# Kernel optimization log

Measured on AMD Instinct MI355X. Metric: run time of the kernel, lower is better.

## Reference

```python
import jax, jax.numpy as jnp
import numpy as np

K = 3          # B-spline order (cubic)
G = 10         # number of spline intervals over [0, 1]
NELY, NELX = 512, 512
WIDTHS = [2, 32, 32, 1]


def _make_grid(in_dim):
    # extended uniform knot vector over [0,1] with K extra knots each side: (in_dim, G+2K+1)
    h = 1.0 / G
    knots = jnp.arange(-K, G + K + 1, dtype=jnp.float32) * h
    return jnp.tile(knots[None, :], (in_dim, 1))


def setup_inputs() -> dict:
    key = jax.random.key(0)
    ks = jax.random.split(key, 1 + 3 * (len(WIDTHS) - 1))
    inp = {"coords": jax.random.uniform(ks[0], (NELY * NELX, 2), dtype=jnp.float32)}
    for l, (i, o) in enumerate(zip(WIDTHS[:-1], WIDTHS[1:])):
        inp[f"grid{l}"] = _make_grid(i)
        inp[f"coef{l}"] = 0.1 * jax.random.normal(ks[1 + 3 * l], (i, o, G + K), dtype=jnp.float32)
        inp[f"sb{l}"] = jax.random.normal(ks[2 + 3 * l], (i, o), dtype=jnp.float32) / np.sqrt(i).astype(np.float32)
        inp[f"sp{l}"] = jnp.ones((i, o), dtype=jnp.float32)
    inp["density_bias"] = jnp.full((1,), np.float32(np.log(0.5 / (1.0 - 0.5 + 1e-8))))
    return inp


def _b_batch(x, grid):
    # Cox-de Boor recursion. x: (B, in), grid: (in, G+2K+1) -> bases (B, in, G+K)
    xe = x[:, :, None]
    v = ((xe >= grid[None, :, :-1]) & (xe < grid[None, :, 1:])).astype(x.dtype)
    for p in range(1, K + 1):
        left = (xe - grid[None, :, : -(p + 1)]) / (grid[None, :, p:-1] - grid[None, :, : -(p + 1)])
        right = (grid[None, :, p + 1:] - xe) / (grid[None, :, p + 1:] - grid[None, :, 1:-p])
        v = left * v[:, :, :-1] + right * v[:, :, 1:]
    return v


def _kan_layer(x, grid, coef, sb, sp):
    # y_out = sum_in [ sb * silu(x) + sp * sum_k B_k(x) * coef_k ]
    B = _b_batch(x, grid)                               # (batch, in, G+K)
    spline = jnp.einsum('bik,iok->bio', B, coef)        # (batch, in, out)
    base = jax.nn.silu(x)                               # (batch, in)
    return jnp.sum(sb[None] * base[:, :, None] + sp[None] * spline, axis=1)


def reference(coords, grid0, coef0, sb0, sp0, grid1, coef1, sb1, sp1,
              grid2, coef2, sb2, sp2, density_bias):
    h = _kan_layer(coords, grid0, coef0, sb0, sp0)
    h = _kan_layer(h, grid1, coef1, sb1, sp1)
    logits = _kan_layer(h, grid2, coef2, sb2, sp2) + density_bias
    return jax.nn.sigmoid(logits).reshape(1, NELY, NELX)
```

## Files before the change

### kernel.cpp

```cpp
#include <hip/hip_runtime.h>
#include <hip/hip_bf16.h>

typedef __hip_bfloat16 bf16;
typedef __fp16 h2v __attribute__((ext_vector_type(2)));
typedef __fp16 half8 __attribute__((ext_vector_type(8)));
typedef float floatx4 __attribute__((ext_vector_type(4)));

#define NPTS (512*512)

#define OFF_BIAS 12
#define OFF_FLAG 13
#define OFF_BF   16
#define NFRAG    50
#define WS_WORDS (16 + NFRAG*64*4)


__device__ __forceinline__ bool sniff_f32(const void* g0) {
    float f = ((const float*)g0)[0];
    return fabsf(f + 0.3f) < 0.01f;
}
__device__ __forceinline__ float ld(const void* p, int i, bool f32) {
    return f32 ? ((const float*)p)[i] : __bfloat162float(((const bf16*)p)[i]);
}
__device__ __forceinline__ unsigned pk_rtn(float a, float b) {
    union { h2v v; unsigned u; } x;
    x.v[0] = (__fp16)a; x.v[1] = (__fp16)b;
    return x.u;
}
__device__ __forceinline__ unsigned pkf16(float a, float b) {
    union { h2v v; unsigned u; } x;
    x.v = __builtin_amdgcn_cvt_pkrtz(a, b);
    return x.u;
}

__device__ float slotval(int layer, int K, int o,
                         const void* c0, const void* sb0, const void* sp0,
                         const void* c1, const void* sb1, const void* sp1,
                         const void* c2, const void* sb2, const void* sp2, bool f32)
{
    int i = K >> 4, s = K & 15;
    if (layer == 2 && o != 0) return 0.0f;
    if (s >= 1 && s <= 13) {
        int m = s - 1;
        if (layer == 0) return ld(c0, (i*32+o)*13 + m, f32) * ld(sp0, i*32+o, f32);
        if (layer == 1) return ld(c1, (i*32+o)*13 + m, f32) * ld(sp1, i*32+o, f32);
        return ld(c2, i*13 + m, f32) * ld(sp2, i, f32);
    }
    if (s == 14) {
        if (layer == 0) return ld(sb0, i*32+o, f32);
        if (layer == 1) return ld(sb1, i*32+o, f32);
        return ld(sb2, i, f32);
    }
    return 0.0f;
}

__global__ __launch_bounds__(256) void kan_prep(
    const void* __restrict__ g0, const void* __restrict__ c0,
    const void* __restrict__ sb0, const void* __restrict__ sp0,
    const void* __restrict__ g1, const void* __restrict__ c1,
    const void* __restrict__ sb1, const void* __restrict__ sp1,
    const void* __restrict__ g2, const void* __restrict__ c2,
    const void* __restrict__ sb2, const void* __restrict__ sp2,
    const void* __restrict__ bias, float* __restrict__ ws)
{
    const bool f32 = sniff_f32(g0);
    int t = blockIdx.x * blockDim.x + threadIdx.x;

    if (t < 16) {
        if (t < 12) {
            int l = t >> 2, j = t & 3;
            const void* g = (l == 0) ? g0 : (l == 1) ? g1 : g2;
            float lo = ld(g, 0, f32), hi = ld(g, 16, f32);
            float ih = 16.0f / (hi - lo);
            float v = (j == 0) ? lo : (j == 1) ? hi
                    : (j == 2) ? ih : (-lo * ih);
            ws[t] = v;
        } else if (t == 12) ws[12] = ld(bias, 0, f32);
        else if (t == 13)   ws[13] = f32 ? 1.0f : 0.0f;
        else                ws[t] = 0.0f;
        return;
    }
    int ft = t - 16;
    if (ft >= NFRAG * 64) return;
    int f = ft >> 6, l = ft & 63, n = l & 15, q = l >> 4;
    int layer, c, nt;
    if (f < 2)       { layer = 0; c = 0;          nt = f; }
    else if (f < 34) { layer = 1; c = (f - 2) >> 1; nt = (f - 2) & 1; }
    else             { layer = 2; c = f - 34;     nt = 0; }
    int o = nt * 16 + n;
    unsigned wv[4];
#pragma unroll
    for (int jp = 0; jp < 4; jp++) {
        int K0 = c * 32 + q * 8 + jp * 2;
        float v0 = slotval(layer, K0,     o, c0,sb0,sp0, c1,sb1,sp1, c2,sb2,sp2, f32);
        float v1 = slotval(layer, K0 + 1, o, c0,sb0,sp0, c1,sb1,sp1, c2,sb2,sp2, f32);
        wv[jp] = pk_rtn(v0, v1);
    }
    uint4 out4; out4.x = wv[0]; out4.y = wv[1]; out4.z = wv[2]; out4.w = wv[3];
    ((uint4*)((unsigned*)ws + OFF_BF))[f * 64 + l] = out4;
}

__device__ __forceinline__ floatx4 mf(uint4 a, uint4 b, floatx4 c)
{
    union { uint4 u; half8 h; } ua, ub;
    ua.u = a; ub.u = b;
    return __builtin_amdgcn_mfma_f32_16x16x32_f16(ua.h, ub.h, c, 0, 0, 0);
}

__device__ __forceinline__ void eval_taps(float x, float ngh, float ih,
    unsigned& A, unsigned& B, unsigned& C, int& wout, float& si)
{
    float t  = fmaf(x, ih, ngh);
    float fj = floorf(t);
    float u  = t - fj;
    bool inb = (t >= 0.0f) && (t < 16.0f);
    float s6 = inb ? 0.166666667f : 0.0f;
    int jc = min(max((int)fj, 0), 15);
    float u2 = u * u, u3 = u2 * u, om = 1.0f - u;
    float b0 = om * om * om * s6;
    float b1 = (fmaf(3.0f, u3, 4.0f) - 6.0f * u2) * s6;
    float b2 = fmaf(-3.0f, u3, fmaf(3.0f, u2, fmaf(3.0f, u, 1.0f))) * s6;
    float b3 = u3 * s6;
    int s0 = jc - 2;
    wout = ((s0 + 2) >> 1) - 1;
    if (s0 & 1) { A = pkf16(0.0f, b0); B = pkf16(b1, b2); C = pkf16(b3, 0.0f); }
    else        { A = pkf16(b0, b1);   B = pkf16(b2, b3); C = 0u; }
    si = x / (1.0f + __expf(-x));
}

__device__ __forceinline__ void stage2(unsigned* row, float f0, float f1,
                                       float ngh, float ih)
{
    uint4 z; z.x = 0u; z.y = 0u; z.z = 0u; z.w = 0u;
    *(uint4*)(row + 0)  = z;
    *(uint4*)(row + 4)  = z;
    *(uint4*)(row + 8)  = z;
    *(uint4*)(row + 12) = z;
    unsigned A0,B0,C0,A1,B1,C1; int w0,w1; float s0,s1;
    eval_taps(f0, ngh, ih, A0, B0, C0, w0, s0);
    eval_taps(f1, ngh, ih, A1, B1, C1, w1, s1);
    row[w0]     = A0; row[w0 + 1]  = B0; row[w0 + 2]  = C0;
    row[8 + w1] = A1; row[9 + w1]  = B1; row[10 + w1] = C1;
    row[7]  = pkf16(s0, 0.0f);
    row[15] = pkf16(s1, 0.0f);
}

__global__ __launch_bounds__(256, 4) void kan_main(
    const void* __restrict__ coords, const float* __restrict__ ws,
    void* __restrict__ out)
{
    __shared__ __align__(16) unsigned lds[4 * 1280];
    const unsigned* wsu = (const unsigned*)ws;
    const uint4* bfp = (const uint4*)(wsu + OFF_BF);

    int tid = threadIdx.x;
    int l = tid & 63, w = tid >> 6;
    int p = blockIdx.x * 256 + w * 64 + l;

    unsigned* rb = lds + w * 1280;
    unsigned* cb = rb;
    unsigned* myrow = cb + l * 20;

    const bool f32 = (ws[OFF_FLAG] != 0.0f);
    float x0, x1;
    if (f32) {
        float2 c = ((const float2*)coords)[p];
        x0 = c.x; x1 = c.y;
    } else {
        unsigned cc = ((const unsigned*)coords)[p];
        union { unsigned u; float f; } cv;
        cv.u = (cc & 0xffffu) << 16;  x0 = cv.f;
        cv.u = cc & 0xffff0000u;      x1 = cv.f;
    }

    const float iha = ws[2],  ngha = ws[3];
    const float ihb = ws[6],  nghb = ws[7];
    const float ihc = ws[10], nghc = ws[11];

    const int arow = l & 15, aq = (l >> 4) * 4;
    const int drow = (l >> 4) * 4, dcol = l & 15;

    float h[32];

    {
        floatx4 acc[4][2];
#pragma unroll
        for (int mt = 0; mt < 4; mt++)
#pragma unroll
            for (int nt = 0; nt < 2; nt++) acc[mt][nt] = (floatx4)0.0f;

        uint4 bf0 = bfp[0 * 64 + l], bf1 = bfp[1 * 64 + l];
        stage2(myrow, x0, x1, ngha, iha);
#pragma unroll
        for (int mt = 0; mt < 4; mt++) {
            uint4 a = *(const uint4*)(cb + (arow + 16 * mt) * 20 + aq);
            acc[mt][0] = mf(a, bf0, acc[mt][0]);
            acc[mt][1] = mf(a, bf1, acc[mt][1]);
        }
#pragma unroll
        for (int nt = 0; nt < 2; nt++) {
#pragma unroll
            for (int mt = 0; mt < 4; mt++)
#pragma unroll
                for (int r = 0; r < 4; r++)
                    rb[(mt*16 + drow + r) * 20 + dcol] =
                        __float_as_uint(acc[mt][nt][r]);
#pragma unroll
            for (int q = 0; q < 4; q++) {
                uint4 v = *(const uint4*)(rb + l * 20 + q * 4);
                h[nt*16 + q*4+0] = __uint_as_float(v.x);
                h[nt*16 + q*4+1] = __uint_as_float(v.y);
                h[nt*16 + q*4+2] = __uint_as_float(v.z);
                h[nt*16 + q*4+3] = __uint_as_float(v.w);
            }
        }
    }

    {
        floatx4 acc[4][2];
#pragma unroll
        for (int mt = 0; mt < 4; mt++)
#pragma unroll
            for (int nt = 0; nt < 2; nt++) acc[mt][nt] = (floatx4)0.0f;

#pragma unroll
        for (int c = 0; c < 16; c++) {
            uint4 bf0 = bfp[(2 + 2*c) * 64 + l];
            uint4 bf1 = bfp[(3 + 2*c) * 64 + l];
            stage2(myrow, h[2*c], h[2*c + 1], nghb, ihb);
#pragma unroll
            for (int mt = 0; mt < 4; mt++) {
                uint4 a = *(const uint4*)(cb + (arow + 16 * mt) * 20 + aq);
                acc[mt][0] = mf(a, bf0, acc[mt][0]);
                acc[mt][1] = mf(a, bf1, acc[mt][1]);
            }
        }
#pragma unroll
        for (int nt = 0; nt < 2; nt++) {
#pragma unroll
            for (int mt = 0; mt < 4; mt++)
#pragma unroll
                for (int r = 0; r < 4; r++)
                    rb[(mt*16 + drow + r) * 20 + dcol] =
                        __float_as_uint(acc[mt][nt][r]);
#pragma unroll
            for (int q = 0; q < 4; q++) {
                uint4 v = *(const uint4*)(rb + l * 20 + q * 4);
                h[nt*16 + q*4+0] = __uint_as_float(v.x);
                h[nt*16 + q*4+1] = __uint_as_float(v.y);
                h[nt*16 + q*4+2] = __uint_as_float(v.z);
                h[nt*16 + q*4+3] = __uint_as_float(v.w);
            }
        }
    }

    {
        floatx4 acc[4];
#pragma unroll
        for (int mt = 0; mt < 4; mt++) acc[mt] = (floatx4)0.0f;

#pragma unroll
        for (int c = 0; c < 16; c++) {
            uint4 bf = bfp[(34 + c) * 64 + l];
            stage2(myrow, h[2*c], h[2*c + 1], nghc, ihc);
#pragma unroll
            for (int mt = 0; mt < 4; mt++) {
                uint4 a = *(const uint4*)(cb + (arow + 16 * mt) * 20 + aq);
                acc[mt] = mf(a, bf, acc[mt]);
            }
        }
        if ((l & 15) == 0) {
#pragma unroll
            for (int mt = 0; mt < 4; mt++)
#pragma unroll
                for (int r = 0; r < 4; r++)
                    rb[(mt*16 + drow + r) * 20] = __float_as_uint(acc[mt][r]);
        }
        float z = __uint_as_float(rb[l * 20]);
        float r = 1.0f / (1.0f + __expf(-(z + ws[OFF_BIAS])));
        if (f32) ((float*)out)[p] = r;
        else     ((bf16*)out)[p] = __float2bfloat16(r);
    }
}

extern "C" void kernel_launch(void* const* d_in, const int* in_sizes, int n_in,
                              void* d_out, int out_size, void* d_ws, size_t ws_size,
                              hipStream_t stream)
{
    float* ws = (float*)d_ws;

    kan_prep<<<(16 + NFRAG*64 + 255) / 256, 256, 0, stream>>>(
        d_in[1], d_in[2], d_in[3], d_in[4],
        d_in[5], d_in[6], d_in[7], d_in[8],
        d_in[9], d_in[10], d_in[11], d_in[12],
        d_in[13], ws);

    kan_main<<<NPTS / 256, 256, 0, stream>>>(d_in[0], ws, d_out);
}
```

Before: 121.1 us.

## Software-pipeline spline tap evaluation and weight loads ahead of MFMA chunks

Splits the per-chunk stage into a register-only tap evaluation and an LDS commit. In layers two and three, the next chunk's basis taps and B-fragment loads are computed before the current chunk's MFMAs issue, and committed afterwards. This lets VALU work and global loads overlap matrix-core work instead of running serially. It costs extra live registers under a 4-wave occupancy bound, and it adds a guard that redirects negative tap indices.

Result: no change. 121.0 us (-0.1%).

```diff
diff --git a/kernel.cpp b/kernel.cpp
--- a/kernel.cpp
+++ b/kernel.cpp
@@ -128,21 +128,38 @@
     si = x / (1.0f + __expf(-x));
 }
 
-__device__ __forceinline__ void stage2(unsigned* row, float f0, float f1,
-                                       float ngh, float ih)
+struct TapPack {
+    unsigned A0, B0, C0, A1, B1, C1, S0, S1;
+    int w0, w1;
+};
+
+__device__ __forceinline__ TapPack eval2(float f0, float f1,
+                                         float ngh, float ih)
+{
+    TapPack t;
+    float si0, si1;
+    eval_taps(f0, ngh, ih, t.A0, t.B0, t.C0, t.w0, si0);
+    eval_taps(f1, ngh, ih, t.A1, t.B1, t.C1, t.w1, si1);
+    t.S0 = pkf16(si0, 0.0f);
+    t.S1 = pkf16(si1, 0.0f);
+    return t;
+}
+
+__device__ __forceinline__ void commit(unsigned* row, const TapPack& t)
 {
     uint4 z; z.x = 0u; z.y = 0u; z.z = 0u; z.w = 0u;
     *(uint4*)(row + 0)  = z;
     *(uint4*)(row + 4)  = z;
     *(uint4*)(row + 8)  = z;
     *(uint4*)(row + 12) = z;
-    unsigned A0,B0,C0,A1,B1,C1; int w0,w1; float s0,s1;
-    eval_taps(f0, ngh, ih, A0, B0, C0, w0, s0);
-    eval_taps(f1, ngh, ih, A1, B1, C1, w1, s1);
-    row[w0]     = A0; row[w0 + 1]  = B0; row[w0 + 2]  = C0;
-    row[8 + w1] = A1; row[9 + w1]  = B1; row[10 + w1] = C1;
-    row[7]  = pkf16(s0, 0.0f);
-    row[15] = pkf16(s1, 0.0f);
+    row[t.w0 < 0 ? 18 : t.w0] = t.A0;
+    row[t.w0 + 1]  = t.B0;
+    row[t.w0 + 2]  = t.C0;
+    row[8 + t.w1]  = t.A1;
+    row[9 + t.w1]  = t.B1;
+    row[10 + t.w1] = t.C1;
+    row[7]  = t.S0;
+    row[15] = t.S1;
 }
 
 __global__ __launch_bounds__(256, 4) void kan_main(
@@ -190,7 +207,8 @@
             for (int nt = 0; nt < 2; nt++) acc[mt][nt] = (floatx4)0.0f;
 
         uint4 bf0 = bfp[0 * 64 + l], bf1 = bfp[1 * 64 + l];
-        stage2(myrow, x0, x1, ngha, iha);
+        TapPack t0 = eval2(x0, x1, ngha, iha);
+        commit(myrow, t0);
 #pragma unroll
         for (int mt = 0; mt < 4; mt++) {
             uint4 a = *(const uint4*)(cb + (arow + 16 * mt) * 20 + aq);
@@ -223,17 +241,26 @@
 #pragma unroll
             for (int nt = 0; nt < 2; nt++) acc[mt][nt] = (floatx4)0.0f;
 
+        uint4 bf0 = bfp[2 * 64 + l], bf1 = bfp[3 * 64 + l];
+        {
+            TapPack t0 = eval2(h[0], h[1], nghb, ihb);
+            commit(myrow, t0);
+        }
 #pragma unroll
         for (int c = 0; c < 16; c++) {
-            uint4 bf0 = bfp[(2 + 2*c) * 64 + l];
-            uint4 bf1 = bfp[(3 + 2*c) * 64 + l];
-            stage2(myrow, h[2*c], h[2*c + 1], nghb, ihb);
+            uint4 nbf0, nbf1; TapPack tn;
+            if (c < 15) {
+                nbf0 = bfp[(4 + 2*c) * 64 + l];
+                nbf1 = bfp[(5 + 2*c) * 64 + l];
+                tn = eval2(h[2*c + 2], h[2*c + 3], nghb, ihb);
+            }
 #pragma unroll
             for (int mt = 0; mt < 4; mt++) {
                 uint4 a = *(const uint4*)(cb + (arow + 16 * mt) * 20 + aq);
                 acc[mt][0] = mf(a, bf0, acc[mt][0]);
                 acc[mt][1] = mf(a, bf1, acc[mt][1]);
             }
+            if (c < 15) { commit(myrow, tn); bf0 = nbf0; bf1 = nbf1; }
         }
 #pragma unroll
         for (int nt = 0; nt < 2; nt++) {
@@ -259,15 +286,24 @@
 #pragma unroll
         for (int mt = 0; mt < 4; mt++) acc[mt] = (floatx4)0.0f;
 
+        uint4 bf = bfp[34 * 64 + l];
+        {
+            TapPack t0 = eval2(h[0], h[1], nghc, ihc);
+            commit(myrow, t0);
+        }
 #pragma unroll
         for (int c = 0; c < 16; c++) {
-            uint4 bf = bfp[(34 + c) * 64 + l];
-            stage2(myrow, h[2*c], h[2*c + 1], nghc, ihc);
+            uint4 nbf; TapPack tn;
+            if (c < 15) {
+                nbf = bfp[(35 + c) * 64 + l];
+                tn = eval2(h[2*c + 2], h[2*c + 3], nghc, ihc);
+            }
 #pragma unroll
             for (int mt = 0; mt < 4; mt++) {
                 uint4 a = *(const uint4*)(cb + (arow + 16 * mt) * 20 + aq);
                 acc[mt] = mf(a, bf, acc[mt]);
             }
+            if (c < 15) { commit(myrow, tn); bf = nbf; }
         }
         if ((l & 15) == 0) {
 #pragma unroll
```
